# Optimization experiments

Measured on AMD Instinct MI355X. Metric: run time of the kernel, lower is better.

Reference implementation:

```python
import jax, jax.numpy as jnp
import numpy as np

HEADS = 16
DIM_HEAD = 64
SCALE = DIM_HEAD ** -0.5
MASK_NEG = 1000000.0


def setup_inputs() -> dict:
    key = jax.random.key(0)
    ks = jax.random.split(key, 6)
    B, N, M, D = 2, 2048, 2048, 1024
    inner = HEADS * DIM_HEAD  # 1024
    x = jax.random.normal(ks[0], (B, N, D), dtype=jnp.float32)
    context = jax.random.normal(ks[1], (B, M, D), dtype=jnp.float32)
    mask = jax.random.randint(ks[2], (B, N), 0, 2, dtype=jnp.int32)
    Wq = jax.random.normal(ks[3], (D, inner), dtype=jnp.float32) * (D ** -0.5)
    Wkv = jax.random.normal(ks[4], (D, 2 * inner), dtype=jnp.float32) * (D ** -0.5)
    Wout = jax.random.normal(ks[5], (inner, D), dtype=jnp.float32) * (inner ** -0.5)
    bout = jnp.zeros((D,), dtype=jnp.float32)
    return {"x": x, "context": context, "mask": mask,
            "Wq": Wq, "Wkv": Wkv, "Wout": Wout, "bout": bout}


def _split_heads(t):
    # [b, n, (h d)] -> [b, h, n, d]
    b, n, _ = t.shape
    return t.reshape(b, n, HEADS, DIM_HEAD).transpose(0, 2, 1, 3)


def reference(x, context, mask, Wq, Wkv, Wout, bout):
    kv = context @ Wkv                      # [b, m, 2*inner]
    k, v = jnp.split(kv, 2, axis=-1)
    q = x @ Wq                              # [b, n, inner]
    q, k, v = _split_heads(q), _split_heads(k), _split_heads(v)
    dots = jnp.einsum('bhnd,bhmd->bhnm', q, k) * SCALE
    # mask is [b, n]: additive penalty per query row (faithful to source)
    dots = dots - (1.0 - mask.astype(jnp.float32))[:, None, :, None] * MASK_NEG
    attn = jax.nn.softmax(dots, axis=-1)
    out = jnp.einsum('bhnm,bhmd->bhnd', attn, v)  # [b, h, n, d]
    b, h, n, d = out.shape
    out = out.transpose(0, 2, 1, 3).reshape(b, n, h * d)
    return out @ Wout + bout
```

## Files before the change

### kernel.cpp

```cpp
#include <hip/hip_runtime.h>
#include <hip/hip_bf16.h>
#include <math.h>

#define BATCH   2
#define NQ      2048
#define NKV     2048
#define DMODEL  1024
#define HEADS   16
#define INNER   1024
#define KVCOLS  2048

typedef short bf16x8 __attribute__((ext_vector_type(8)));
typedef float f32x4  __attribute__((ext_vector_type(4)));

__device__ __forceinline__ short f2bf(float x) {
    __hip_bfloat16 h = __float2bfloat16(x);
    return *reinterpret_cast<short*>(&h);
}
__device__ __forceinline__ float bf2f(short h) {
    unsigned int u = ((unsigned int)(unsigned short)h) << 16;
    float f;
    __builtin_memcpy(&f, &u, 4);
    return f;
}
__device__ __forceinline__ void gl_lds16(const void* g, void* l) {
    __builtin_amdgcn_global_load_lds(
        (const __attribute__((address_space(1))) unsigned int*)g,
        (__attribute__((address_space(3))) unsigned int*)l, 16, 0, 0);
}
__device__ __forceinline__ int sw(int row, int chunk) {
    return row * 64 + ((chunk ^ (row & 7)) << 3);
}

__device__ __forceinline__ void split_chunk(const float* __restrict__ in,
                                            short* __restrict__ hi,
                                            short* __restrict__ lo, int id)
{
    const int i = (id * 256 + (int)threadIdx.x) * 4;
    float4 v = *(const float4*)(in + i);
    short4 h, l;
    h.x = f2bf(v.x); l.x = f2bf(v.x - bf2f(h.x));
    h.y = f2bf(v.y); l.y = f2bf(v.y - bf2f(h.y));
    h.z = f2bf(v.z); l.z = f2bf(v.z - bf2f(h.z));
    h.w = f2bf(v.w); l.w = f2bf(v.w - bf2f(h.w));
    *(short4*)(hi + i) = h;
    *(short4*)(lo + i) = l;
}

__device__ __forceinline__ void tile_transpose_split(
    const float* __restrict__ W, short* __restrict__ Wth, short* __restrict__ Wtl,
    int Kd, int Nd, int bx, int by, int split)
{
    __shared__ float t[32][33];
    const int lx = threadIdx.x & 31, ly = threadIdx.x >> 5;
    #pragma unroll
    for (int j = 0; j < 4; ++j)
        t[ly + j * 8][lx] = W[(size_t)(by * 32 + ly + j * 8) * Nd + bx * 32 + lx];
    __syncthreads();
    #pragma unroll
    for (int j = 0; j < 4; ++j) {
        const float v = t[lx][ly + j * 8];
        const short h = f2bf(v);
        const size_t idx = (size_t)(bx * 32 + ly + j * 8) * Kd + by * 32 + lx;
        Wth[idx] = h;
        if (split) Wtl[idx] = f2bf(v - bf2f(h));
    }
}

__global__ __launch_bounds__(256)
void prep_all(const float* __restrict__ x, const float* __restrict__ ctx,
              const float* __restrict__ Wq, const float* __restrict__ Wkv,
              const float* __restrict__ Wout,
              short* __restrict__ xh, short* __restrict__ xl,
              short* __restrict__ ch, short* __restrict__ cl,
              short* __restrict__ WqTh, short* __restrict__ WqTl,
              short* __restrict__ WkvTh, short* __restrict__ WkvTl,
              short* __restrict__ WoutT)
{
    const int id = blockIdx.x;
    if (id < 4096) {
        split_chunk(x, xh, xl, id);
    } else if (id < 8192) {
        split_chunk(ctx, ch, cl, id - 4096);
    } else {
        const int r = id - 8192;
        if (r < 1024)
            tile_transpose_split(Wq, WqTh, WqTl, 1024, 1024, r & 31, r >> 5, 1);
        else if (r < 3072)
            tile_transpose_split(Wkv, WkvTh, WkvTl, 1024, 2048, (r - 1024) & 63, (r - 1024) >> 6, 1);
        else
            tile_transpose_split(Wout, WoutT, nullptr, 1024, 1024, (r - 3072) & 31, (r - 3072) >> 5, 0);
    }
}

__global__ __launch_bounds__(256)
void qkv_gemm(const short* __restrict__ xh, const short* __restrict__ xl,
              const short* __restrict__ ch, const short* __restrict__ cl,
              const short* __restrict__ WqTh, const short* __restrict__ WqTl,
              const short* __restrict__ WkvTh, const short* __restrict__ WkvTl,
              short* __restrict__ qhp, short* __restrict__ qlp,
              short* __restrict__ khp, short* __restrict__ klp,
              short* __restrict__ vp)
{
    __shared__ short Ash[128 * 32];
    __shared__ short Asl[128 * 32];
    __shared__ short Bsh[128 * 32];
    __shared__ short Bsl[128 * 32];

    const int tid = threadIdx.x;
    const int z = blockIdx.z;
    const int m0 = blockIdx.y * 128, n0 = blockIdx.x * 128;
    const int w = tid >> 6, ln = tid & 63;
    const int wm = (w & 1) * 64, wn = (w >> 1) * 64;
    const int lr = ln & 15, lq = ln >> 4;
    const int terms = (z == 2) ? 1 : 3;

    const short* Ah  = (z == 0) ? xh : ch;
    const short* Al  = (z == 0) ? xl : cl;
    const short* Bth = (z == 0) ? WqTh : (z == 1 ? WkvTh : WkvTh + (size_t)1024 * 1024);
    const short* Btl = (z == 0) ? WqTl : WkvTl;

    f32x4 acc[4][4];
    #pragma unroll
    for (int mt = 0; mt < 4; ++mt)
        #pragma unroll
        for (int nt = 0; nt < 4; ++nt)
            #pragma unroll
            for (int r = 0; r < 4; ++r) acc[mt][nt][r] = 0.0f;

    for (int k0 = 0; k0 < 1024; k0 += 32) {
        __syncthreads();
        #pragma unroll
        for (int it = 0; it < 2; ++it) {
            const int f = it * 256 + tid;
            const int row = f >> 2, c = f & 3;
            const int cg = c ^ ((row >> 1) & 3);
            const size_t ao = (size_t)(m0 + row) * 1024 + k0 + cg * 8;
            const size_t bo = (size_t)(n0 + row) * 1024 + k0 + cg * 8;
            gl_lds16(Ah  + ao, Ash + f * 8);
            gl_lds16(Bth + bo, Bsh + f * 8);
            if (terms == 3) {
                gl_lds16(Al  + ao, Asl + f * 8);
                gl_lds16(Btl + bo, Bsl + f * 8);
            }
        }
        __syncthreads();

        bf16x8 ah[4], bh[4];
        #pragma unroll
        for (int t = 0; t < 4; ++t) {
            const int ar = wm + t * 16 + lr;
            const int br = wn + t * 16 + lr;
            ah[t] = *(const bf16x8*)(Ash + ar * 32 + ((lq ^ ((ar >> 1) & 3)) << 3));
            bh[t] = *(const bf16x8*)(Bsh + br * 32 + ((lq ^ ((br >> 1) & 3)) << 3));
        }
        #pragma unroll
        for (int mt = 0; mt < 4; ++mt)
            #pragma unroll
            for (int nt = 0; nt < 4; ++nt)
                acc[mt][nt] = __builtin_amdgcn_mfma_f32_16x16x32_bf16(
                    ah[mt], bh[nt], acc[mt][nt], 0, 0, 0);

        if (terms == 3) {
            bf16x8 al[4], bl[4];
            #pragma unroll
            for (int t = 0; t < 4; ++t) {
                const int ar = wm + t * 16 + lr;
                const int br = wn + t * 16 + lr;
                al[t] = *(const bf16x8*)(Asl + ar * 32 + ((lq ^ ((ar >> 1) & 3)) << 3));
                bl[t] = *(const bf16x8*)(Bsl + br * 32 + ((lq ^ ((br >> 1) & 3)) << 3));
            }
            #pragma unroll
            for (int mt = 0; mt < 4; ++mt)
                #pragma unroll
                for (int nt = 0; nt < 4; ++nt) {
                    acc[mt][nt] = __builtin_amdgcn_mfma_f32_16x16x32_bf16(
                        ah[mt], bl[nt], acc[mt][nt], 0, 0, 0);
                    acc[mt][nt] = __builtin_amdgcn_mfma_f32_16x16x32_bf16(
                        al[mt], bh[nt], acc[mt][nt], 0, 0, 0);
                }
        }
    }

    const float scale = (z == 0) ? 2.0f : 1.0f;
    short* Chi = (z == 0) ? qhp : (z == 1 ? khp : vp);
    short* Clo = (z == 0) ? qlp : klp;
    #pragma unroll
    for (int mt = 0; mt < 4; ++mt)
        #pragma unroll
        for (int nt = 0; nt < 4; ++nt)
            #pragma unroll
            for (int r = 0; r < 4; ++r) {
                const int row = m0 + wm + mt * 16 + lq * 4 + r;
                const int col = n0 + wn + nt * 16 + lr;
                const float v = acc[mt][nt][r] * scale;
                const short hh = f2bf(v);
                Chi[(size_t)row * 1024 + col] = hh;
                if (z != 2)
                    Clo[(size_t)row * 1024 + col] = f2bf(v - bf2f(hh));
            }
}

__global__ __launch_bounds__(256)
void gemm_out(const short* __restrict__ A, const short* __restrict__ Bt,
              float* __restrict__ C, const float* __restrict__ bias)
{
    __shared__ short As[128 * 64];
    __shared__ short Bs[64 * 64];
    const int tid = threadIdx.x;
    const int m0 = blockIdx.y * 128, n0 = blockIdx.x * 64;
    const int w = tid >> 6, ln = tid & 63;
    const int wm = (w & 1) * 64, wn = (w >> 1) * 32;
    const int lr = ln & 15, lq = ln >> 4;

    f32x4 acc[4][2];
    #pragma unroll
    for (int mt = 0; mt < 4; ++mt)
        #pragma unroll
        for (int nt = 0; nt < 2; ++nt)
            #pragma unroll
            for (int r = 0; r < 4; ++r) acc[mt][nt][r] = 0.0f;

    for (int k0 = 0; k0 < 1024; k0 += 64) {
        __syncthreads();
        #pragma unroll
        for (int it = 0; it < 4; ++it) {
            const int f = it * 256 + tid;
            const int row = f >> 3, c8 = f & 7;
            const int cg = c8 ^ (row & 7);
            gl_lds16(A + (size_t)(m0 + row) * 1024 + k0 + cg * 8, As + f * 8);
        }
        #pragma unroll
        for (int it = 0; it < 2; ++it) {
            const int f = it * 256 + tid;
            const int row = f >> 3, c8 = f & 7;
            const int cg = c8 ^ (row & 7);
            gl_lds16(Bt + (size_t)(n0 + row) * 1024 + k0 + cg * 8, Bs + f * 8);
        }
        __syncthreads();
        #pragma unroll
        for (int ks = 0; ks < 2; ++ks) {
            bf16x8 af[4], bfr[2];
            #pragma unroll
            for (int t = 0; t < 4; ++t) {
                const int ar = wm + t * 16 + lr;
                af[t] = *(const bf16x8*)(As + ar * 64 + (((ks * 4 + lq) ^ (ar & 7)) << 3));
            }
            #pragma unroll
            for (int t = 0; t < 2; ++t) {
                const int br = wn + t * 16 + lr;
                bfr[t] = *(const bf16x8*)(Bs + br * 64 + (((ks * 4 + lq) ^ (br & 7)) << 3));
            }
            #pragma unroll
            for (int mt = 0; mt < 4; ++mt)
                #pragma unroll
                for (int nt = 0; nt < 2; ++nt)
                    acc[mt][nt] = __builtin_amdgcn_mfma_f32_16x16x32_bf16(
                        af[mt], bfr[nt], acc[mt][nt], 0, 0, 0);
        }
    }
    #pragma unroll
    for (int mt = 0; mt < 4; ++mt)
        #pragma unroll
        for (int nt = 0; nt < 2; ++nt)
            #pragma unroll
            for (int r = 0; r < 4; ++r) {
                const int row = m0 + wm + mt * 16 + lq * 4 + r;
                const int col = n0 + wn + nt * 16 + lr;
                C[(size_t)row * 1024 + col] = acc[mt][nt][r] + bias[col];
            }
}

__global__ __launch_bounds__(512, 4)
void flash_v7(const short* __restrict__ qh, const short* __restrict__ ql,
              const short* __restrict__ kh, const short* __restrict__ kl,
              const short* __restrict__ vp, const int* __restrict__ mask,
              short* __restrict__ aob)
{
    const int qt = blockIdx.x, h = blockIdx.y, b = blockIdx.z;
    const int tid = threadIdx.x;
    const int w = tid >> 6, ln = tid & 63;
    const int lr = ln & 15, lq = ln >> 4;

    __shared__ short Kh[2 * 4096];
    __shared__ short Kl[2 * 4096];
    __shared__ short Vt[2 * 4096];
    __shared__ short Ps[128 * 64];

    const size_t qrow0 = (size_t)(b * NQ + qt * 128);

    bf16x8 aqh[2], aql[2];
    #pragma unroll
    for (int ks = 0; ks < 2; ++ks) {
        const size_t qoff = (qrow0 + w * 16 + lr) * INNER + h * 64 + ks * 32 + lq * 8;
        aqh[ks] = *(const bf16x8*)(qh + qoff);
        aql[ks] = *(const bf16x8*)(ql + qoff);
    }
    float bmag[4];
    #pragma unroll
    for (int r = 0; r < 4; ++r)
        bmag[r] = mask[b * NQ + qt * 128 + w * 16 + lq * 4 + r] ? 0.0f : 12582912.0f;

    bf16x8 vone;
    #pragma unroll
    for (int j = 0; j < 8; ++j) vone[j] = (short)0x3F80;

    const int krow = tid >> 3, kc = tid & 7;
    const int kcg = kc ^ (krow & 7);
    const size_t koff0 = ((size_t)(b * NKV + krow)) * INNER + h * 64 + kcg * 8;

    const int idx = tid & 31, dg4 = (tid >> 5) * 4;
    const int vj  = (idx & 15) + ((idx >> 4) << 5);
    const int kp32 = (idx & 15) * 2 + (idx >> 4);
    int2 rva, rvb;

    {
        const short* v0 = vp + (size_t)(b * NKV + vj) * INNER + h * 64 + dg4;
        rva = *(const int2*)(v0);
        rvb = *(const int2*)(v0 + 16 * INNER);
        gl_lds16(kh + koff0, Kh + tid * 8);
        gl_lds16(kl + koff0, Kl + tid * 8);
        const short* as = (const short*)&rva;
        const short* bs = (const short*)&rvb;
        int* vt32 = (int*)Vt;
        #pragma unroll
        for (int j = 0; j < 4; ++j)
            vt32[(dg4 + j) * 32 + (((kp32 >> 2) ^ ((dg4 + j) & 7)) << 2) + (kp32 & 3)] =
                (int)((unsigned short)as[j] | ((unsigned int)(unsigned short)bs[j] << 16));
    }

    f32x4 oacc[4];
    #pragma unroll
    for (int dg = 0; dg < 4; ++dg)
        #pragma unroll
        for (int r = 0; r < 4; ++r) oacc[dg][r] = 0.0f;
    f32x4 pacc;
    #pragma unroll
    for (int r = 0; r < 4; ++r) pacc[r] = 0.0f;

    const float C16 = 1.44269504f * 0.0625f;

    for (int kt = 0; kt < NKV / 64; ++kt) {
        const int cur = kt & 1;
        __syncthreads();

        if (kt < NKV / 64 - 1) {
            const size_t krow0 = (size_t)(b * NKV + (kt + 1) * 64);
            const short* v0 = vp + (krow0 + vj) * INNER + h * 64 + dg4;
            rva = *(const int2*)(v0);
            rvb = *(const int2*)(v0 + 16 * INNER);
            const int nb = (cur ^ 1) * 4096;
            const size_t kadd = (size_t)((kt + 1) * 64) * INNER;
            gl_lds16(kh + koff0 + kadd, Kh + nb + tid * 8);
            gl_lds16(kl + koff0 + kadd, Kl + nb + tid * 8);
        }

        const short* KhC = Kh + cur * 4096;
        const short* KlC = Kl + cur * 4096;
        const short* VtC = Vt + cur * 4096;

        f32x4 sacc[4];
        #pragma unroll
        for (int g = 0; g < 4; ++g)
            #pragma unroll
            for (int r = 0; r < 4; ++r) sacc[g][r] = 0.0f;
        #pragma unroll
        for (int ks = 0; ks < 2; ++ks) {
            #pragma unroll
            for (int g = 0; g < 4; ++g) {
                const bf16x8 bkh = *(const bf16x8*)(KhC + sw(g * 16 + lr, ks * 4 + lq));
                const bf16x8 bkl = *(const bf16x8*)(KlC + sw(g * 16 + lr, ks * 4 + lq));
                sacc[g] = __builtin_amdgcn_mfma_f32_16x16x32_bf16(aqh[ks], bkh, sacc[g], 0, 0, 0);
                sacc[g] = __builtin_amdgcn_mfma_f32_16x16x32_bf16(aqh[ks], bkl, sacc[g], 0, 0, 0);
                sacc[g] = __builtin_amdgcn_mfma_f32_16x16x32_bf16(aql[ks], bkh, sacc[g], 0, 0, 0);
            }
        }

        #pragma unroll
        for (int r = 0; r < 4; ++r) {
            const int prow = w * 16 + lq * 4 + r;
            short4 pw;
            #pragma unroll
            for (int g = 0; g < 4; ++g) {
                const float sq = (sacc[g][r] + bmag[r]) - bmag[r];
                const float xx = sq * C16;
                float pv;
                asm("v_exp_f32 %0, %1" : "=v"(pv) : "v"(xx));
                ((short*)&pw)[g] = f2bf(pv);
            }
            *(short4*)(Ps + sw(prow, lr >> 1) + (lr & 1) * 4) = pw;
        }

        #pragma unroll
        for (int ks = 0; ks < 2; ++ks) {
            const bf16x8 ap = *(const bf16x8*)(Ps + sw(w * 16 + lr, ks * 4 + lq));
            pacc = __builtin_amdgcn_mfma_f32_16x16x32_bf16(ap, vone, pacc, 0, 0, 0);
            #pragma unroll
            for (int dg = 0; dg < 4; ++dg) {
                const bf16x8 bv = *(const bf16x8*)(VtC + sw(dg * 16 + lr, ks * 4 + lq));
                oacc[dg] = __builtin_amdgcn_mfma_f32_16x16x32_bf16(ap, bv, oacc[dg], 0, 0, 0);
            }
        }

        if (kt < NKV / 64 - 1) {
            const short* as = (const short*)&rva;
            const short* bs = (const short*)&rvb;
            int* vt32 = (int*)(Vt + (cur ^ 1) * 4096);
            #pragma unroll
            for (int j = 0; j < 4; ++j)
                vt32[(dg4 + j) * 32 + (((kp32 >> 2) ^ ((dg4 + j) & 7)) << 2) + (kp32 & 3)] =
                    (int)((unsigned short)as[j] | ((unsigned int)(unsigned short)bs[j] << 16));
        }
    }

    float pinv[4];
    #pragma unroll
    for (int r = 0; r < 4; ++r) pinv[r] = 1.0f / pacc[r];

    #pragma unroll
    for (int dg = 0; dg < 4; ++dg)
        #pragma unroll
        for (int r = 0; r < 4; ++r) {
            const int row = w * 16 + lq * 4 + r;
            aob[(qrow0 + row) * INNER + h * 64 + dg * 16 + lr] =
                f2bf(oacc[dg][r] * pinv[r]);
        }
}

extern "C" void kernel_launch(void* const* d_in, const int* in_sizes, int n_in,
                              void* d_out, int out_size, void* d_ws, size_t ws_size,
                              hipStream_t stream)
{
    const float* x    = (const float*)d_in[0];
    const float* ctx  = (const float*)d_in[1];
    const int*   mask = (const int*)d_in[2];
    const float* Wq   = (const float*)d_in[3];
    const float* Wkv  = (const float*)d_in[4];
    const float* Wout = (const float*)d_in[5];
    const float* bout = (const float*)d_in[6];
    float* out = (float*)d_out;

    short* base  = (short*)d_ws;
    short* xh    = base;
    short* xl    = base + (size_t)4 * 1024 * 1024;
    short* aob   = xh;
    short* WqTh  = base + (size_t) 8 * 1024 * 1024;
    short* WqTl  = base + (size_t) 9 * 1024 * 1024;
    short* qhp   = base + (size_t)10 * 1024 * 1024;
    short* qlp   = base + (size_t)14 * 1024 * 1024;
    short* WkvTh = base + (size_t)18 * 1024 * 1024;
    short* WkvTl = base + (size_t)20 * 1024 * 1024;
    short* khp   = base + (size_t)22 * 1024 * 1024;
    short* klp   = base + (size_t)26 * 1024 * 1024;
    short* WoutT = base + (size_t)30 * 1024 * 1024;
    short* ch    = base + (size_t)31 * 1024 * 1024;
    short* cl    = base + (size_t)35 * 1024 * 1024;
    short* vp    = base + (size_t)39 * 1024 * 1024;

    const dim3 blk(256);
    prep_all<<<12288, blk, 0, stream>>>(x, ctx, Wq, Wkv, Wout,
                                        xh, xl, ch, cl,
                                        WqTh, WqTl, WkvTh, WkvTl, WoutT);
    qkv_gemm<<<dim3(8, 32, 3), blk, 0, stream>>>(
        xh, xl, ch, cl, WqTh, WqTl, WkvTh, WkvTl,
        qhp, qlp, khp, klp, vp);
    flash_v7<<<dim3(NQ / 128, HEADS, BATCH), dim3(512), 0, stream>>>(
        qhp, qlp, khp, klp, vp, mask, aob);
    gemm_out<<<dim3(1024 / 64, 4096 / 128), blk, 0, stream>>>(
        aob, WoutT, out, bout);
}
```

Before: 259.7 us.

## Halve flash-attention block to 4 waves, each handling two 16-row query tiles

The attention kernel now launches 256 threads per block instead of 512. Each wave processes 32 query rows as two 16-row MFMA tiles, so every K and V fragment read from LDS feeds two MFMAs. Each thread issues twice as many K/V global-to-LDS loads to fill the same 64-row tiles. This roughly halves LDS reads per MFMA, but doubles accumulator registers per thread and halves the wave count available for latency hiding.

```diff
diff --git a/kernel.cpp b/kernel.cpp
--- a/kernel.cpp
+++ b/kernel.cpp
@@ -271,8 +271,19 @@
             }
 }
 
-__global__ __launch_bounds__(512, 4)
-void flash_v7(const short* __restrict__ qh, const short* __restrict__ ql,
+__device__ __forceinline__ void vwrite(int* __restrict__ vt32, int dg4, int kp32,
+                                       int2 a, int2 b)
+{
+    const short* as = (const short*)&a;
+    const short* bs = (const short*)&b;
+    #pragma unroll
+    for (int j = 0; j < 4; ++j)
+        vt32[(dg4 + j) * 32 + (((kp32 >> 2) ^ ((dg4 + j) & 7)) << 2) + (kp32 & 3)] =
+            (int)((unsigned short)as[j] | ((unsigned int)(unsigned short)bs[j] << 16));
+}
+
+__global__ __launch_bounds__(256, 2)
+void flash_v8(const short* __restrict__ qh, const short* __restrict__ ql,
               const short* __restrict__ kh, const short* __restrict__ kl,
               const short* __restrict__ vp, const int* __restrict__ mask,
               short* __restrict__ aob)
@@ -289,54 +300,70 @@
 
     const size_t qrow0 = (size_t)(b * NQ + qt * 128);
 
-    bf16x8 aqh[2], aql[2];
-    #pragma unroll
-    for (int ks = 0; ks < 2; ++ks) {
-        const size_t qoff = (qrow0 + w * 16 + lr) * INNER + h * 64 + ks * 32 + lq * 8;
-        aqh[ks] = *(const bf16x8*)(qh + qoff);
-        aql[ks] = *(const bf16x8*)(ql + qoff);
-    }
-    float bmag[4];
-    #pragma unroll
-    for (int r = 0; r < 4; ++r)
-        bmag[r] = mask[b * NQ + qt * 128 + w * 16 + lq * 4 + r] ? 0.0f : 12582912.0f;
+    bf16x8 aqh[2][2], aql[2][2];
+    #pragma unroll
+    for (int m = 0; m < 2; ++m)
+        #pragma unroll
+        for (int ks = 0; ks < 2; ++ks) {
+            const size_t qoff = (qrow0 + w * 32 + m * 16 + lr) * INNER + h * 64 + ks * 32 + lq * 8;
+            aqh[m][ks] = *(const bf16x8*)(qh + qoff);
+            aql[m][ks] = *(const bf16x8*)(ql + qoff);
+        }
+    float bmag[2][4];
+    #pragma unroll
+    for (int m = 0; m < 2; ++m)
+        #pragma unroll
+        for (int r = 0; r < 4; ++r)
+            bmag[m][r] = mask[b * NQ + qt * 128 + w * 32 + m * 16 + lq * 4 + r]
+                         ? 0.0f : 12582912.0f;
 
     bf16x8 vone;
     #pragma unroll
     for (int j = 0; j < 8; ++j) vone[j] = (short)0x3F80;
 
-    const int krow = tid >> 3, kc = tid & 7;
-    const int kcg = kc ^ (krow & 7);
-    const size_t koff0 = ((size_t)(b * NKV + krow)) * INNER + h * 64 + kcg * 8;
-
-    const int idx = tid & 31, dg4 = (tid >> 5) * 4;
+    size_t koff[2];
+    #pragma unroll
+    for (int it = 0; it < 2; ++it) {
+        const int f = it * 256 + tid;
+        const int krow = f >> 3, kc = f & 7;
+        const int kcg = kc ^ (krow & 7);
+        koff[it] = ((size_t)(b * NKV + krow)) * INNER + h * 64 + kcg * 8;
+    }
+
+    const int idx = tid & 31;
     const int vj  = (idx & 15) + ((idx >> 4) << 5);
     const int kp32 = (idx & 15) * 2 + (idx >> 4);
-    int2 rva, rvb;
+    const int dgA = (tid >> 5) * 4;
+    const int dgB = dgA + 32;
+    int2 rva, rvb, rvc, rvd;
 
     {
-        const short* v0 = vp + (size_t)(b * NKV + vj) * INNER + h * 64 + dg4;
-        rva = *(const int2*)(v0);
-        rvb = *(const int2*)(v0 + 16 * INNER);
-        gl_lds16(kh + koff0, Kh + tid * 8);
-        gl_lds16(kl + koff0, Kl + tid * 8);
-        const short* as = (const short*)&rva;
-        const short* bs = (const short*)&rvb;
+        const short* v0 = vp + (size_t)(b * NKV + vj) * INNER + h * 64;
+        rva = *(const int2*)(v0 + dgA);
+        rvb = *(const int2*)(v0 + dgA + 16 * INNER);
+        rvc = *(const int2*)(v0 + dgB);
+        rvd = *(const int2*)(v0 + dgB + 16 * INNER);
+        gl_lds16(kh + koff[0], Kh + tid * 8);
+        gl_lds16(kh + koff[1], Kh + 2048 + tid * 8);
+        gl_lds16(kl + koff[0], Kl + tid * 8);
+        gl_lds16(kl + koff[1], Kl + 2048 + tid * 8);
         int* vt32 = (int*)Vt;
-        #pragma unroll
-        for (int j = 0; j < 4; ++j)
-            vt32[(dg4 + j) * 32 + (((kp32 >> 2) ^ ((dg4 + j) & 7)) << 2) + (kp32 & 3)] =
-                (int)((unsigned short)as[j] | ((unsigned int)(unsigned short)bs[j] << 16));
-    }
-
-    f32x4 oacc[4];
-    #pragma unroll
-    for (int dg = 0; dg < 4; ++dg)
-        #pragma unroll
-        for (int r = 0; r < 4; ++r) oacc[dg][r] = 0.0f;
-    f32x4 pacc;
-    #pragma unroll
-    for (int r = 0; r < 4; ++r) pacc[r] = 0.0f;
+        vwrite(vt32, dgA, kp32, rva, rvb);
+        vwrite(vt32, dgB, kp32, rvc, rvd);
+    }
+
+    f32x4 oacc[2][4];
+    #pragma unroll
+    for (int m = 0; m < 2; ++m)
+        #pragma unroll
+        for (int dg = 0; dg < 4; ++dg)
+            #pragma unroll
+            for (int r = 0; r < 4; ++r) oacc[m][dg][r] = 0.0f;
+    f32x4 pacc[2];
+    #pragma unroll
+    for (int m = 0; m < 2; ++m)
+        #pragma unroll
+        for (int r = 0; r < 4; ++r) pacc[m][r] = 0.0f;
 
     const float C16 = 1.44269504f * 0.0625f;
 
@@ -345,86 +372,99 @@
         __syncthreads();
 
         if (kt < NKV / 64 - 1) {
-            const size_t krow0 = (size_t)(b * NKV + (kt + 1) * 64);
-            const short* v0 = vp + (krow0 + vj) * INNER + h * 64 + dg4;
-            rva = *(const int2*)(v0);
-            rvb = *(const int2*)(v0 + 16 * INNER);
+            const size_t kadd = (size_t)((kt + 1) * 64) * INNER;
+            const short* v0 = vp + (size_t)(b * NKV + (kt + 1) * 64 + vj) * INNER + h * 64;
+            rva = *(const int2*)(v0 + dgA);
+            rvb = *(const int2*)(v0 + dgA + 16 * INNER);
+            rvc = *(const int2*)(v0 + dgB);
+            rvd = *(const int2*)(v0 + dgB + 16 * INNER);
             const int nb = (cur ^ 1) * 4096;
-            const size_t kadd = (size_t)((kt + 1) * 64) * INNER;
-            gl_lds16(kh + koff0 + kadd, Kh + nb + tid * 8);
-            gl_lds16(kl + koff0 + kadd, Kl + nb + tid * 8);
+            gl_lds16(kh + koff[0] + kadd, Kh + nb + tid * 8);
+            gl_lds16(kh + koff[1] + kadd, Kh + nb + 2048 + tid * 8);
+            gl_lds16(kl + koff[0] + kadd, Kl + nb + tid * 8);
+            gl_lds16(kl + koff[1] + kadd, Kl + nb + 2048 + tid * 8);
         }
 
         const short* KhC = Kh + cur * 4096;
         const short* KlC = Kl + cur * 4096;
         const short* VtC = Vt + cur * 4096;
 
-        f32x4 sacc[4];
-        #pragma unroll
-        for (int g = 0; g < 4; ++g)
-            #pragma unroll
-            for (int r = 0; r < 4; ++r) sacc[g][r] = 0.0f;
+        f32x4 sacc[2][4];
+        #pragma unroll
+        for (int m = 0; m < 2; ++m)
+            #pragma unroll
+            for (int g = 0; g < 4; ++g)
+                #pragma unroll
+                for (int r = 0; r < 4; ++r) sacc[m][g][r] = 0.0f;
         #pragma unroll
         for (int ks = 0; ks < 2; ++ks) {
             #pragma unroll
             for (int g = 0; g < 4; ++g) {
                 const bf16x8 bkh = *(const bf16x8*)(KhC + sw(g * 16 + lr, ks * 4 + lq));
                 const bf16x8 bkl = *(const bf16x8*)(KlC + sw(g * 16 + lr, ks * 4 + lq));
-                sacc[g] = __builtin_amdgcn_mfma_f32_16x16x32_bf16(aqh[ks], bkh, sacc[g], 0, 0, 0);
-                sacc[g] = __builtin_amdgcn_mfma_f32_16x16x32_bf16(aqh[ks], bkl, sacc[g], 0, 0, 0);
-                sacc[g] = __builtin_amdgcn_mfma_f32_16x16x32_bf16(aql[ks], bkh, sacc[g], 0, 0, 0);
-            }
-        }
-
-        #pragma unroll
-        for (int r = 0; r < 4; ++r) {
-            const int prow = w * 16 + lq * 4 + r;
-            short4 pw;
-            #pragma unroll
-            for (int g = 0; g < 4; ++g) {
-                const float sq = (sacc[g][r] + bmag[r]) - bmag[r];
-                const float xx = sq * C16;
-                float pv;
-                asm("v_exp_f32 %0, %1" : "=v"(pv) : "v"(xx));
-                ((short*)&pw)[g] = f2bf(pv);
-            }
-            *(short4*)(Ps + sw(prow, lr >> 1) + (lr & 1) * 4) = pw;
-        }
+                #pragma unroll
+                for (int m = 0; m < 2; ++m) {
+                    sacc[m][g] = __builtin_amdgcn_mfma_f32_16x16x32_bf16(aqh[m][ks], bkh, sacc[m][g], 0, 0, 0);
+                    sacc[m][g] = __builtin_amdgcn_mfma_f32_16x16x32_bf16(aqh[m][ks], bkl, sacc[m][g], 0, 0, 0);
+                    sacc[m][g] = __builtin_amdgcn_mfma_f32_16x16x32_bf16(aql[m][ks], bkh, sacc[m][g], 0, 0, 0);
+                }
+            }
+        }
+
+        #pragma unroll
+        for (int m = 0; m < 2; ++m)
+            #pragma unroll
+            for (int r = 0; r < 4; ++r) {
+                const int prow = w * 32 + m * 16 + lq * 4 + r;
+                short4 pw;
+                #pragma unroll
+                for (int g = 0; g < 4; ++g) {
+                    const float sq = (sacc[m][g][r] + bmag[m][r]) - bmag[m][r];
+                    const float xx = sq * C16;
+                    float pv;
+                    asm("v_exp_f32 %0, %1" : "=v"(pv) : "v"(xx));
+                    ((short*)&pw)[g] = f2bf(pv);
+                }
+                *(short4*)(Ps + sw(prow, lr >> 1) + (lr & 1) * 4) = pw;
+            }
 
         #pragma unroll
         for (int ks = 0; ks < 2; ++ks) {
-            const bf16x8 ap = *(const bf16x8*)(Ps + sw(w * 16 + lr, ks * 4 + lq));
-            pacc = __builtin_amdgcn_mfma_f32_16x16x32_bf16(ap, vone, pacc, 0, 0, 0);
+            bf16x8 ap[2];
+            #pragma unroll
+            for (int m = 0; m < 2; ++m) {
+                ap[m] = *(const bf16x8*)(Ps + sw(w * 32 + m * 16 + lr, ks * 4 + lq));
+                pacc[m] = __builtin_amdgcn_mfma_f32_16x16x32_bf16(ap[m], vone, pacc[m], 0, 0, 0);
+            }
             #pragma unroll
             for (int dg = 0; dg < 4; ++dg) {
                 const bf16x8 bv = *(const bf16x8*)(VtC + sw(dg * 16 + lr, ks * 4 + lq));
-                oacc[dg] = __builtin_amdgcn_mfma_f32_16x16x32_bf16(ap, bv, oacc[dg], 0, 0, 0);
+                oacc[0][dg] = __builtin_amdgcn_mfma_f32_16x16x32_bf16(ap[0], bv, oacc[0][dg], 0, 0, 0);
+                oacc[1][dg] = __builtin_amdgcn_mfma_f32_16x16x32_bf16(ap[1], bv, oacc[1][dg], 0, 0, 0);
             }
         }
 
         if (kt < NKV / 64 - 1) {
-            const short* as = (const short*)&rva;
-            const short* bs = (const short*)&rvb;
             int* vt32 = (int*)(Vt + (cur ^ 1) * 4096);
-            #pragma unroll
-            for (int j = 0; j < 4; ++j)
-                vt32[(dg4 + j) * 32 + (((kp32 >> 2) ^ ((dg4 + j) & 7)) << 2) + (kp32 & 3)] =
-                    (int)((unsigned short)as[j] | ((unsigned int)(unsigned short)bs[j] << 16));
-        }
-    }
-
-    float pinv[4];
-    #pragma unroll
-    for (int r = 0; r < 4; ++r) pinv[r] = 1.0f / pacc[r];
-
-    #pragma unroll
-    for (int dg = 0; dg < 4; ++dg)
-        #pragma unroll
-        for (int r = 0; r < 4; ++r) {
-            const int row = w * 16 + lq * 4 + r;
-            aob[(qrow0 + row) * INNER + h * 64 + dg * 16 + lr] =
-                f2bf(oacc[dg][r] * pinv[r]);
-        }
+            vwrite(vt32, dgA, kp32, rva, rvb);
+            vwrite(vt32, dgB, kp32, rvc, rvd);
+        }
+    }
+
+    #pragma unroll
+    for (int m = 0; m < 2; ++m) {
+        float pinv[4];
+        #pragma unroll
+        for (int r = 0; r < 4; ++r) pinv[r] = 1.0f / pacc[m][r];
+        #pragma unroll
+        for (int dg = 0; dg < 4; ++dg)
+            #pragma unroll
+            for (int r = 0; r < 4; ++r) {
+                const int row = w * 32 + m * 16 + lq * 4 + r;
+                aob[(qrow0 + row) * INNER + h * 64 + dg * 16 + lr] =
+                    f2bf(oacc[m][dg][r] * pinv[r]);
+            }
+    }
 }
 
 extern "C" void kernel_launch(void* const* d_in, const int* in_sizes, int n_in,
@@ -464,7 +504,7 @@
     qkv_gemm<<<dim3(8, 32, 3), blk, 0, stream>>>(
         xh, xl, ch, cl, WqTh, WqTl, WkvTh, WkvTl,
         qhp, qlp, khp, klp, vp);
-    flash_v7<<<dim3(NQ / 128, HEADS, BATCH), dim3(512), 0, stream>>>(
+    flash_v8<<<dim3(NQ / 128, HEADS, BATCH), dim3(256), 0, stream>>>(
         qhp, qlp, khp, klp, vp, mask, aob);
     gemm_out<<<dim3(1024 / 64, 4096 / 128), blk, 0, stream>>>(
         aob, WoutT, out, bout);
```

Result: slower. 270.0 us (+3.9%).

## Compute transposed S so P stays in registers, dropping LDS P round-trip

Applied to the files above, without the earlier changes.

The QK^T MFMA operands are swapped so each lane holds scores in the layout the PV MFMA needs as its A operand. The P tile is packed directly into bf16 registers instead of being written to and reloaded from a shared-memory buffer. To make this work, the V loading permutes key order and the mask is indexed per lane. s_setprio hints are also added around the MFMA blocks. This removes LDS traffic and shared memory use, but the remapped key order must stay consistent or results will be wrong.

```diff
diff --git a/kernel.cpp b/kernel.cpp
--- a/kernel.cpp
+++ b/kernel.cpp
@@ -271,11 +271,22 @@
             }
 }
 
+__device__ __forceinline__ void vwrite(int* __restrict__ vt32, int dg4, int slot,
+                                       int2 a, int2 b)
+{
+    const short* as = (const short*)&a;
+    const short* bs = (const short*)&b;
+    #pragma unroll
+    for (int j = 0; j < 4; ++j)
+        vt32[(dg4 + j) * 32 + (((slot >> 2) ^ ((dg4 + j) & 7)) << 2) + (slot & 3)] =
+            (int)((unsigned short)as[j] | ((unsigned int)(unsigned short)bs[j] << 16));
+}
+
 __global__ __launch_bounds__(512, 4)
-void flash_v7(const short* __restrict__ qh, const short* __restrict__ ql,
-              const short* __restrict__ kh, const short* __restrict__ kl,
-              const short* __restrict__ vp, const int* __restrict__ mask,
-              short* __restrict__ aob)
+void flash_v10(const short* __restrict__ qh, const short* __restrict__ ql,
+               const short* __restrict__ kh, const short* __restrict__ kl,
+               const short* __restrict__ vp, const int* __restrict__ mask,
+               short* __restrict__ aob)
 {
     const int qt = blockIdx.x, h = blockIdx.y, b = blockIdx.z;
     const int tid = threadIdx.x;
@@ -285,7 +296,6 @@
     __shared__ short Kh[2 * 4096];
     __shared__ short Kl[2 * 4096];
     __shared__ short Vt[2 * 4096];
-    __shared__ short Ps[128 * 64];
 
     const size_t qrow0 = (size_t)(b * NQ + qt * 128);
 
@@ -296,10 +306,7 @@
         aqh[ks] = *(const bf16x8*)(qh + qoff);
         aql[ks] = *(const bf16x8*)(ql + qoff);
     }
-    float bmag[4];
-    #pragma unroll
-    for (int r = 0; r < 4; ++r)
-        bmag[r] = mask[b * NQ + qt * 128 + w * 16 + lq * 4 + r] ? 0.0f : 12582912.0f;
+    const float bmag = mask[b * NQ + qt * 128 + w * 16 + lr] ? 0.0f : 12582912.0f;
 
     bf16x8 vone;
     #pragma unroll
@@ -310,23 +317,18 @@
     const size_t koff0 = ((size_t)(b * NKV + krow)) * INNER + h * 64 + kcg * 8;
 
     const int idx = tid & 31, dg4 = (tid >> 5) * 4;
-    const int vj  = (idx & 15) + ((idx >> 4) << 5);
-    const int kp32 = (idx & 15) * 2 + (idx >> 4);
+    const int tp = idx & 15;
+    const int vkey = ((tp >> 2) << 2) + 2 * (tp & 1) + (((tp >> 1) & 1) << 4)
+                   + ((idx >> 4) << 5);
     int2 rva, rvb;
 
     {
-        const short* v0 = vp + (size_t)(b * NKV + vj) * INNER + h * 64 + dg4;
+        const short* v0 = vp + (size_t)(b * NKV + vkey) * INNER + h * 64 + dg4;
         rva = *(const int2*)(v0);
-        rvb = *(const int2*)(v0 + 16 * INNER);
+        rvb = *(const int2*)(v0 + INNER);
         gl_lds16(kh + koff0, Kh + tid * 8);
         gl_lds16(kl + koff0, Kl + tid * 8);
-        const short* as = (const short*)&rva;
-        const short* bs = (const short*)&rvb;
-        int* vt32 = (int*)Vt;
-        #pragma unroll
-        for (int j = 0; j < 4; ++j)
-            vt32[(dg4 + j) * 32 + (((kp32 >> 2) ^ ((dg4 + j) & 7)) << 2) + (kp32 & 3)] =
-                (int)((unsigned short)as[j] | ((unsigned int)(unsigned short)bs[j] << 16));
+        vwrite((int*)Vt, dg4, idx, rva, rvb);
     }
 
     f32x4 oacc[4];
@@ -345,12 +347,11 @@
         __syncthreads();
 
         if (kt < NKV / 64 - 1) {
-            const size_t krow0 = (size_t)(b * NKV + (kt + 1) * 64);
-            const short* v0 = vp + (krow0 + vj) * INNER + h * 64 + dg4;
+            const size_t kadd = (size_t)((kt + 1) * 64) * INNER;
+            const short* v0 = vp + (size_t)(b * NKV + (kt + 1) * 64 + vkey) * INNER + h * 64 + dg4;
             rva = *(const int2*)(v0);
-            rvb = *(const int2*)(v0 + 16 * INNER);
+            rvb = *(const int2*)(v0 + INNER);
             const int nb = (cur ^ 1) * 4096;
-            const size_t kadd = (size_t)((kt + 1) * 64) * INNER;
             gl_lds16(kh + koff0 + kadd, Kh + nb + tid * 8);
             gl_lds16(kl + koff0 + kadd, Kl + nb + tid * 8);
         }
@@ -364,52 +365,51 @@
         for (int g = 0; g < 4; ++g)
             #pragma unroll
             for (int r = 0; r < 4; ++r) sacc[g][r] = 0.0f;
+        __builtin_amdgcn_s_setprio(1);
         #pragma unroll
         for (int ks = 0; ks < 2; ++ks) {
             #pragma unroll
             for (int g = 0; g < 4; ++g) {
                 const bf16x8 bkh = *(const bf16x8*)(KhC + sw(g * 16 + lr, ks * 4 + lq));
                 const bf16x8 bkl = *(const bf16x8*)(KlC + sw(g * 16 + lr, ks * 4 + lq));
-                sacc[g] = __builtin_amdgcn_mfma_f32_16x16x32_bf16(aqh[ks], bkh, sacc[g], 0, 0, 0);
-                sacc[g] = __builtin_amdgcn_mfma_f32_16x16x32_bf16(aqh[ks], bkl, sacc[g], 0, 0, 0);
-                sacc[g] = __builtin_amdgcn_mfma_f32_16x16x32_bf16(aql[ks], bkh, sacc[g], 0, 0, 0);
-            }
-        }
-
-        #pragma unroll
-        for (int r = 0; r < 4; ++r) {
-            const int prow = w * 16 + lq * 4 + r;
-            short4 pw;
-            #pragma unroll
-            for (int g = 0; g < 4; ++g) {
-                const float sq = (sacc[g][r] + bmag[r]) - bmag[r];
-                const float xx = sq * C16;
-                float pv;
-                asm("v_exp_f32 %0, %1" : "=v"(pv) : "v"(xx));
-                ((short*)&pw)[g] = f2bf(pv);
-            }
-            *(short4*)(Ps + sw(prow, lr >> 1) + (lr & 1) * 4) = pw;
-        }
-
+                sacc[g] = __builtin_amdgcn_mfma_f32_16x16x32_bf16(bkh, aqh[ks], sacc[g], 0, 0, 0);
+                sacc[g] = __builtin_amdgcn_mfma_f32_16x16x32_bf16(bkl, aqh[ks], sacc[g], 0, 0, 0);
+                sacc[g] = __builtin_amdgcn_mfma_f32_16x16x32_bf16(bkh, aql[ks], sacc[g], 0, 0, 0);
+            }
+        }
+        __builtin_amdgcn_s_setprio(0);
+
+        bf16x8 ap[2];
         #pragma unroll
         for (int ks = 0; ks < 2; ++ks) {
-            const bf16x8 ap = *(const bf16x8*)(Ps + sw(w * 16 + lr, ks * 4 + lq));
-            pacc = __builtin_amdgcn_mfma_f32_16x16x32_bf16(ap, vone, pacc, 0, 0, 0);
+            bf16x8 a;
+            #pragma unroll
+            for (int g2 = 0; g2 < 2; ++g2)
+                #pragma unroll
+                for (int r = 0; r < 4; ++r) {
+                    const float sq = (sacc[2 * ks + g2][r] + bmag) - bmag;
+                    const float xx = sq * C16;
+                    float pv;
+                    asm("v_exp_f32 %0, %1" : "=v"(pv) : "v"(xx));
+                    a[g2 * 4 + r] = f2bf(pv);
+                }
+            ap[ks] = a;
+        }
+
+        __builtin_amdgcn_s_setprio(1);
+        #pragma unroll
+        for (int ks = 0; ks < 2; ++ks) {
+            pacc = __builtin_amdgcn_mfma_f32_16x16x32_bf16(ap[ks], vone, pacc, 0, 0, 0);
             #pragma unroll
             for (int dg = 0; dg < 4; ++dg) {
                 const bf16x8 bv = *(const bf16x8*)(VtC + sw(dg * 16 + lr, ks * 4 + lq));
-                oacc[dg] = __builtin_amdgcn_mfma_f32_16x16x32_bf16(ap, bv, oacc[dg], 0, 0, 0);
-            }
-        }
+                oacc[dg] = __builtin_amdgcn_mfma_f32_16x16x32_bf16(ap[ks], bv, oacc[dg], 0, 0, 0);
+            }
+        }
+        __builtin_amdgcn_s_setprio(0);
 
         if (kt < NKV / 64 - 1) {
-            const short* as = (const short*)&rva;
-            const short* bs = (const short*)&rvb;
-            int* vt32 = (int*)(Vt + (cur ^ 1) * 4096);
-            #pragma unroll
-            for (int j = 0; j < 4; ++j)
-                vt32[(dg4 + j) * 32 + (((kp32 >> 2) ^ ((dg4 + j) & 7)) << 2) + (kp32 & 3)] =
-                    (int)((unsigned short)as[j] | ((unsigned int)(unsigned short)bs[j] << 16));
+            vwrite((int*)(Vt + (cur ^ 1) * 4096), dg4, idx, rva, rvb);
         }
     }
 
@@ -464,7 +464,7 @@
     qkv_gemm<<<dim3(8, 32, 3), blk, 0, stream>>>(
         xh, xl, ch, cl, WqTh, WqTl, WkvTh, WkvTl,
         qhp, qlp, khp, klp, vp);
-    flash_v7<<<dim3(NQ / 128, HEADS, BATCH), dim3(512), 0, stream>>>(
+    flash_v10<<<dim3(NQ / 128, HEADS, BATCH), dim3(512), 0, stream>>>(
         qhp, qlp, khp, klp, vp, mask, aob);
     gemm_out<<<dim3(1024 / 64, 4096 / 128), blk, 0, stream>>>(
         aob, WoutT, out, bout);
```

Measured after the change: 252.2 us (median of 2 runs). 2.9% less time.
